# Kernel optimization log

Measured on AMD Instinct MI355X. Metric: run time of the kernel, lower is better.

The kernel has to match this reference:

```python
import jax, jax.numpy as jnp
import numpy as np

N_NODES = 50000
N_EDGES = 800000
IN_C, HID_C, OUT_C = 512, 256, 128


def setup_inputs() -> dict:
    key = jax.random.key(0)
    k1, k2, k3, k4, k5, k6 = jax.random.split(key, 6)
    x = jax.random.normal(k1, (N_NODES, IN_C), dtype=jnp.float32)
    edge_index = jax.random.randint(k2, (2, N_EDGES), 0, N_NODES, dtype=jnp.int64)
    # Glorot-ish init for linear weights, zero bias (PyG GCNConv default)
    W1 = jax.random.normal(k3, (IN_C, HID_C), dtype=jnp.float32) / np.sqrt(IN_C)
    b1 = jnp.zeros((HID_C,), dtype=jnp.float32)
    W2 = jax.random.normal(k4, (HID_C, OUT_C), dtype=jnp.float32) / np.sqrt(HID_C)
    b2 = jnp.zeros((OUT_C,), dtype=jnp.float32)
    return {"x": x, "edge_index": edge_index, "W1": W1, "b1": b1, "W2": W2, "b2": b2}


def _gcn_layer(h, src, dst, norm, W, b, n_nodes):
    # h: [N, Fin] -> [N, Fout];  out_i = sum_{j->i} norm_e * (h W)_j + b
    h = h @ W
    msg = h[src] * norm[:, None]            # [E+N, Fout]
    out = jax.ops.segment_sum(msg, dst, num_segments=n_nodes)
    return out + b


def reference(x, edge_index, W1, b1, W2, b2):
    n = x.shape[0]
    loops = jnp.arange(n, dtype=edge_index.dtype)
    src = jnp.concatenate([edge_index[0], loops])  # add self-loops
    dst = jnp.concatenate([edge_index[1], loops])
    # symmetric normalization D^{-1/2} (A+I) D^{-1/2}
    deg = jax.ops.segment_sum(jnp.ones_like(src, dtype=x.dtype), dst, num_segments=n)
    dinv = jax.lax.rsqrt(jnp.maximum(deg, 1.0))
    norm = dinv[src] * dinv[dst]

    h = _gcn_layer(x, src, dst, norm, W1, b1, n)
    h = jax.nn.relu(h)
    # dropout: identity in eval mode (training=False)
    out = _gcn_layer(h, src, dst, norm, W2, b2, n)
    return out
```

## Files before the change

kernel.cpp:

```cpp
#include <hip/hip_runtime.h>
#include <hip/hip_bf16.h>

#define N_NODES 50000
#define N_EDGES 800000
#define IN_C 512
#define HID_C 256
#define OUT_C 128
#define SCAN_BLOCKS 49

typedef short bf16x8 __attribute__((ext_vector_type(8)));
typedef float f32x4 __attribute__((ext_vector_type(4)));
typedef float f32x2 __attribute__((ext_vector_type(2)));

__device__ __forceinline__ float bf2f(unsigned short u) {
    return __uint_as_float(((unsigned)u) << 16);
}
__device__ __forceinline__ unsigned short f2bf(float f) {
    __hip_bfloat16 h = __float2bfloat16(f);
    return *(unsigned short*)&h;
}
__device__ __forceinline__ void acc_fp8x4(int dw, float* a) {
    f32x2 lo = __builtin_amdgcn_cvt_pk_f32_fp8(dw, false);
    f32x2 hi = __builtin_amdgcn_cvt_pk_f32_fp8(dw, true);
    a[0] += lo[0]; a[1] += lo[1]; a[2] += hi[0]; a[3] += hi[1];
}
__device__ __forceinline__ unsigned char f2fp8(float f) {
    return (unsigned char)(__builtin_amdgcn_cvt_pk_fp8_f32(f, 0.0f, 0, false) & 0xff);
}
__device__ __forceinline__ void glds16(const void* gp, void* lp) {
    __builtin_amdgcn_global_load_lds((const __attribute__((address_space(1))) void*)gp,
                                     (__attribute__((address_space(3))) void*)lp, 16, 0, 0);
}

__global__ void zero_counts_kernel(int* __restrict__ counts) {
    int i = blockIdx.x * blockDim.x + threadIdx.x;
    if (i < N_NODES) counts[i] = 0;
}

__global__ void count_kernel(const int* __restrict__ ei, int* __restrict__ counts) {
    int e = blockIdx.x * blockDim.x + threadIdx.x;
    if (e < N_EDGES) atomicAdd(&counts[ei[N_EDGES + e]], 1);
}

__global__ __launch_bounds__(256) void scan_part_kernel(const int* __restrict__ counts,
                                                        int* __restrict__ excl,
                                                        int* __restrict__ bsums) {
    __shared__ int tsum[256];
    const int t = threadIdx.x;
    const int base = blockIdx.x * 1024 + t * 4;
    int v[4];
    int s = 0;
#pragma unroll
    for (int j = 0; j < 4; j++) {
        int idx = base + j;
        v[j] = (idx < N_NODES) ? counts[idx] : 0;
        s += v[j];
    }
    tsum[t] = s;
    __syncthreads();
    for (int off = 1; off < 256; off <<= 1) {
        int add = (t >= off) ? tsum[t - off] : 0;
        __syncthreads();
        tsum[t] += add;
        __syncthreads();
    }
    int run = tsum[t] - s;
#pragma unroll
    for (int j = 0; j < 4; j++) {
        int idx = base + j;
        if (idx < N_NODES) excl[idx] = run;
        run += v[j];
    }
    if (t == 255) bsums[blockIdx.x] = tsum[255];
}

__global__ void scan_sums_kernel(int* __restrict__ bsums) {
    int ln = threadIdx.x;
    int v = (ln < SCAN_BLOCKS) ? bsums[ln] : 0;
    for (int off = 1; off < 64; off <<= 1) {
        int u = __shfl_up(v, off, 64);
        if (ln >= off) v += u;
    }
    int excl = __shfl_up(v, 1, 64);
    if (ln == 0) excl = 0;
    if (ln < SCAN_BLOCKS) bsums[ln] = excl;
}

__global__ void add_dinv_kernel(int* __restrict__ offsets, const int* __restrict__ bsums,
                                int* __restrict__ woff, const int* __restrict__ counts,
                                float* __restrict__ dinv) {
    int i = blockIdx.x * blockDim.x + threadIdx.x;
    if (i < N_NODES) {
        int o = offsets[i] + bsums[i >> 10];
        offsets[i] = o;
        woff[i] = o;
        dinv[i] = rsqrtf(1.0f + (float)counts[i]);
    }
    if (i == 0) offsets[N_NODES] = N_EDGES;
}

__global__ void fill_kernel(const int* __restrict__ ei, int* __restrict__ woff,
                            int* __restrict__ sedge) {
    int e = blockIdx.x * blockDim.x + threadIdx.x;
    if (e < N_EDGES) {
        int s = ei[e];
        int d = ei[N_EDGES + e];
        int pos = atomicAdd(&woff[d], 1);
        sedge[pos] = s;
    }
}

__global__ __launch_bounds__(256) void tcast_kernel(const float* __restrict__ W,
                                                    unsigned short* __restrict__ WT,
                                                    int K, int N) {
    int idx = blockIdx.x * 256 + threadIdx.x;
    int n = idx / K, k = idx - n * K;
    WT[idx] = f2bf(W[(size_t)k * N + n]);
}

__global__ __launch_bounds__(256) void gemm1_fused(const float* __restrict__ x,
                                                   const unsigned short* __restrict__ BT,
                                                   unsigned char* __restrict__ C,
                                                   const float* __restrict__ dinv) {
    __shared__ unsigned short As[2][64 * 32];
    __shared__ unsigned short Bs[2][256 * 32];

    const int tid = threadIdx.x;
    const int w = tid >> 6;
    const int ln = tid & 63;
    const int br = blockIdx.x * 64;

    const int quad = ln >> 4;
    const int l16 = ln & 15;
    const int wc = w * 64;

    const int ar = tid >> 2;
    const int ak = (tid & 3) * 8;

    int arow = br + ar;
    arow = arow < N_NODES ? arow : N_NODES - 1;
    const float* xrow = x + (size_t)arow * IN_C + ak;
    const int brow = (tid >> 2);

    f32x4 acc[4][4];
#pragma unroll
    for (int mt = 0; mt < 4; mt++)
#pragma unroll
        for (int nt = 0; nt < 4; nt++) acc[mt][nt] = (f32x4){0.f, 0.f, 0.f, 0.f};

    {
        float4 v0 = *(const float4*)(xrow);
        float4 v1 = *(const float4*)(xrow + 4);
#pragma unroll
        for (int tt = 0; tt < 4; tt++) {
            const unsigned short* gp = BT + (size_t)(brow + 64 * tt) * IN_C + ak;
            glds16(gp, &Bs[0][tt * 2048 + tid * 8]);
        }
        bf16x8 a8;
        a8[0] = (short)f2bf(v0.x); a8[1] = (short)f2bf(v0.y);
        a8[2] = (short)f2bf(v0.z); a8[3] = (short)f2bf(v0.w);
        a8[4] = (short)f2bf(v1.x); a8[5] = (short)f2bf(v1.y);
        a8[6] = (short)f2bf(v1.z); a8[7] = (short)f2bf(v1.w);
        *(bf16x8*)&As[0][ar * 32 + ak] = a8;
    }
    __syncthreads();

    for (int t = 0; t < 16; t++) {
        const int buf = t & 1;
        const int nxt = buf ^ 1;
        const bool more = t < 15;
        float4 v0, v1;
        if (more) {
            const int kk = (t + 1) * 32;
            v0 = *(const float4*)(xrow + kk);
            v1 = *(const float4*)(xrow + kk + 4);
#pragma unroll
            for (int tt = 0; tt < 4; tt++) {
                const unsigned short* gp = BT + (size_t)(brow + 64 * tt) * IN_C + kk + ak;
                glds16(gp, &Bs[nxt][tt * 2048 + tid * 8]);
            }
        }

        bf16x8 af[4], bfr[4];
#pragma unroll
        for (int mt = 0; mt < 4; mt++)
            af[mt] = *(const bf16x8*)&As[buf][(mt * 16 + l16) * 32 + quad * 8];
#pragma unroll
        for (int nt = 0; nt < 4; nt++)
            bfr[nt] = *(const bf16x8*)&Bs[buf][(wc + nt * 16 + l16) * 32 + quad * 8];
#pragma unroll
        for (int mt = 0; mt < 4; mt++)
#pragma unroll
            for (int nt = 0; nt < 4; nt++)
                acc[mt][nt] = __builtin_amdgcn_mfma_f32_16x16x32_bf16(af[mt], bfr[nt],
                                                                      acc[mt][nt], 0, 0, 0);
        if (more) {
            bf16x8 a8;
            a8[0] = (short)f2bf(v0.x); a8[1] = (short)f2bf(v0.y);
            a8[2] = (short)f2bf(v0.z); a8[3] = (short)f2bf(v0.w);
            a8[4] = (short)f2bf(v1.x); a8[5] = (short)f2bf(v1.y);
            a8[6] = (short)f2bf(v1.z); a8[7] = (short)f2bf(v1.w);
            *(bf16x8*)&As[nxt][ar * 32 + ak] = a8;
        }
        __syncthreads();
    }

#pragma unroll
    for (int mt = 0; mt < 4; mt++) {
#pragma unroll
        for (int r = 0; r < 4; r++) {
            int gr = br + mt * 16 + quad * 4 + r;
            if (gr < N_NODES) {
                float ds = dinv[gr];
#pragma unroll
                for (int nt = 0; nt < 4; nt++) {
                    int gc = wc + nt * 16 + l16;
                    C[(size_t)gr * HID_C + gc] = f2fp8(ds * acc[mt][nt][r]);
                }
            }
        }
    }
}

__global__ __launch_bounds__(256) void gemm2_db(const unsigned short* __restrict__ A,
                                                const unsigned short* __restrict__ BT,
                                                unsigned short* __restrict__ C,
                                                const float* __restrict__ dinv) {
    __shared__ unsigned short As[2][64 * 32];
    __shared__ unsigned short Bs[2][128 * 32];

    const int tid = threadIdx.x;
    const int w = tid >> 6;
    const int ln = tid & 63;
    const int br = blockIdx.x * 64;

    const int quad = ln >> 4;
    const int l16 = ln & 15;
    const int wr = (w >> 1) * 32;
    const int wc = (w & 1) * 64;

    const int ak = (tid & 3) * 8;
    const int trow = tid >> 2;

    int arow = br + trow;
    arow = arow < N_NODES ? arow : N_NODES - 1;
    const unsigned short* agp0 = A + (size_t)arow * HID_C + ak;

    f32x4 acc[2][4];
#pragma unroll
    for (int mt = 0; mt < 2; mt++)
#pragma unroll
        for (int nt = 0; nt < 4; nt++) acc[mt][nt] = (f32x4){0.f, 0.f, 0.f, 0.f};

    glds16(agp0, &As[0][tid * 8]);
#pragma unroll
    for (int tt = 0; tt < 2; tt++) {
        const unsigned short* gp = BT + (size_t)(trow + 64 * tt) * HID_C + ak;
        glds16(gp, &Bs[0][tt * 2048 + tid * 8]);
    }
    __syncthreads();

    for (int t = 0; t < 8; t++) {
        const int buf = t & 1;
        const int nxt = buf ^ 1;
        if (t < 7) {
            const int kk = (t + 1) * 32;
            glds16(agp0 + kk, &As[nxt][tid * 8]);
#pragma unroll
            for (int tt = 0; tt < 2; tt++) {
                const unsigned short* gp = BT + (size_t)(trow + 64 * tt) * HID_C + kk + ak;
                glds16(gp, &Bs[nxt][tt * 2048 + tid * 8]);
            }
        }

        bf16x8 af[2], bfr[4];
#pragma unroll
        for (int mt = 0; mt < 2; mt++)
            af[mt] = *(const bf16x8*)&As[buf][(wr + mt * 16 + l16) * 32 + quad * 8];
#pragma unroll
        for (int nt = 0; nt < 4; nt++)
            bfr[nt] = *(const bf16x8*)&Bs[buf][(wc + nt * 16 + l16) * 32 + quad * 8];
#pragma unroll
        for (int mt = 0; mt < 2; mt++)
#pragma unroll
            for (int nt = 0; nt < 4; nt++)
                acc[mt][nt] = __builtin_amdgcn_mfma_f32_16x16x32_bf16(af[mt], bfr[nt],
                                                                      acc[mt][nt], 0, 0, 0);
        __syncthreads();
    }

#pragma unroll
    for (int mt = 0; mt < 2; mt++) {
#pragma unroll
        for (int r = 0; r < 4; r++) {
            int gr = br + wr + mt * 16 + quad * 4 + r;
            if (gr < N_NODES) {
                float ds = dinv[gr];
#pragma unroll
                for (int nt = 0; nt < 4; nt++) {
                    int gc = wc + nt * 16 + l16;
                    C[(size_t)gr * OUT_C + gc] = f2bf(ds * acc[mt][nt][r]);
                }
            }
        }
    }
}

__global__ __launch_bounds__(256) void gather1_fp8(const int* __restrict__ offsets,
                                                   const int* __restrict__ sedge,
                                                   const unsigned char* __restrict__ H,
                                                   const float* __restrict__ dinv,
                                                   const float* __restrict__ bias,
                                                   unsigned short* __restrict__ out) {
    const int node = blockIdx.x * 4 + (threadIdx.x >> 6);
    if (node >= N_NODES) return;
    const int ln = threadIdx.x & 63;
    const int g = ln >> 5;
    const int l = ln & 31;
    const int c0 = l * 8;

    float acc[8] = {};
    if (g == 0) {
        uint2 d = *(const uint2*)&H[(size_t)node * HID_C + c0];
        acc_fp8x4((int)d.x, acc);
        acc_fp8x4((int)d.y, acc + 4);
    }

    int k = offsets[node] + g;
    const int k1 = offsets[node + 1];
    for (; k + 6 < k1; k += 8) {
        int s0 = sedge[k], s1 = sedge[k + 2], s2 = sedge[k + 4], s3 = sedge[k + 6];
        uint2 d0 = *(const uint2*)&H[(size_t)s0 * HID_C + c0];
        uint2 d1 = *(const uint2*)&H[(size_t)s1 * HID_C + c0];
        uint2 d2 = *(const uint2*)&H[(size_t)s2 * HID_C + c0];
        uint2 d3 = *(const uint2*)&H[(size_t)s3 * HID_C + c0];
        acc_fp8x4((int)d0.x, acc); acc_fp8x4((int)d0.y, acc + 4);
        acc_fp8x4((int)d1.x, acc); acc_fp8x4((int)d1.y, acc + 4);
        acc_fp8x4((int)d2.x, acc); acc_fp8x4((int)d2.y, acc + 4);
        acc_fp8x4((int)d3.x, acc); acc_fp8x4((int)d3.y, acc + 4);
    }
    for (; k < k1; k += 2) {
        int s0 = sedge[k];
        uint2 d0 = *(const uint2*)&H[(size_t)s0 * HID_C + c0];
        acc_fp8x4((int)d0.x, acc);
        acc_fp8x4((int)d0.y, acc + 4);
    }

#pragma unroll
    for (int j = 0; j < 8; j++) acc[j] += __shfl_xor(acc[j], 32, 64);

    if (g == 0) {
        const float di = dinv[node];
        bf16x8 o;
#pragma unroll
        for (int j = 0; j < 8; j++)
            o[j] = (short)f2bf(fmaxf(di * acc[j] + bias[c0 + j], 0.0f));
        *(bf16x8*)&out[(size_t)node * HID_C + c0] = o;
    }
}

__global__ __launch_bounds__(256) void gather2_bf16(const int* __restrict__ offsets,
                                                    const int* __restrict__ sedge,
                                                    const unsigned short* __restrict__ H,
                                                    const float* __restrict__ dinv,
                                                    const float* __restrict__ bias,
                                                    float* __restrict__ out) {
    const int node = blockIdx.x * 4 + (threadIdx.x >> 6);
    if (node >= N_NODES) return;
    const int ln = threadIdx.x & 63;
    const int g = ln >> 4;
    const int l = ln & 15;
    const int c0 = l * 8;

    float acc[8] = {};
    if (g == 0) {
        bf16x8 h = *(const bf16x8*)&H[(size_t)node * OUT_C + c0];
#pragma unroll
        for (int j = 0; j < 8; j++) acc[j] = bf2f((unsigned short)h[j]);
    }

    int k = offsets[node] + g;
    const int k1 = offsets[node + 1];
    for (; k + 12 < k1; k += 16) {
        int s0 = sedge[k], s1 = sedge[k + 4], s2 = sedge[k + 8], s3 = sedge[k + 12];
        bf16x8 h0 = *(const bf16x8*)&H[(size_t)s0 * OUT_C + c0];
        bf16x8 h1 = *(const bf16x8*)&H[(size_t)s1 * OUT_C + c0];
        bf16x8 h2 = *(const bf16x8*)&H[(size_t)s2 * OUT_C + c0];
        bf16x8 h3 = *(const bf16x8*)&H[(size_t)s3 * OUT_C + c0];
#pragma unroll
        for (int j = 0; j < 8; j++) {
            acc[j] += bf2f((unsigned short)h0[j]);
            acc[j] += bf2f((unsigned short)h1[j]);
            acc[j] += bf2f((unsigned short)h2[j]);
            acc[j] += bf2f((unsigned short)h3[j]);
        }
    }
    for (; k < k1; k += 4) {
        int s0 = sedge[k];
        bf16x8 h0 = *(const bf16x8*)&H[(size_t)s0 * OUT_C + c0];
#pragma unroll
        for (int j = 0; j < 8; j++) acc[j] += bf2f((unsigned short)h0[j]);
    }

#pragma unroll
    for (int m = 16; m < 64; m <<= 1) {
#pragma unroll
        for (int j = 0; j < 8; j++) acc[j] += __shfl_xor(acc[j], m, 64);
    }

    if (g == 0) {
        const float di = dinv[node];
        float o[8];
#pragma unroll
        for (int j = 0; j < 8; j++) o[j] = di * acc[j] + bias[c0 + j];
        *(float4*)&out[(size_t)node * OUT_C + c0] = make_float4(o[0], o[1], o[2], o[3]);
        *(float4*)&out[(size_t)node * OUT_C + c0 + 4] = make_float4(o[4], o[5], o[6], o[7]);
    }
}

extern "C" void kernel_launch(void* const* d_in, const int* in_sizes, int n_in,
                              void* d_out, int out_size, void* d_ws, size_t ws_size,
                              hipStream_t stream) {
    const float* x  = (const float*)d_in[0];
    const int*   ei = (const int*)d_in[1];
    const float* W1 = (const float*)d_in[2];
    const float* b1 = (const float*)d_in[3];
    const float* W2 = (const float*)d_in[4];
    const float* b2 = (const float*)d_in[5];
    float* out = (float*)d_out;

    int*   counts     = (int*)d_ws;
    int*   offsets    = counts + 50048;
    int*   woff       = offsets + 50052;
    int*   bsums      = woff + 50048;
    float* dinv       = (float*)(bsums + 64);
    int*   sedge      = (int*)(dinv + 50048);
    unsigned short* W1T = (unsigned short*)(sedge + 800000);
    unsigned short* W2T = W1T + 131072;
    unsigned short* xb  = W2T + 32768;
    unsigned char*  H1  = (unsigned char*)(xb + (size_t)N_NODES * IN_C);
    unsigned short* A1b = xb;
    unsigned short* H2  = xb + (size_t)N_NODES * HID_C;

    zero_counts_kernel<<<(N_NODES + 255) / 256, 256, 0, stream>>>(counts);
    count_kernel<<<(N_EDGES + 255) / 256, 256, 0, stream>>>(ei, counts);
    scan_part_kernel<<<SCAN_BLOCKS, 256, 0, stream>>>(counts, offsets, bsums);
    scan_sums_kernel<<<1, 64, 0, stream>>>(bsums);
    add_dinv_kernel<<<(N_NODES + 255) / 256, 256, 0, stream>>>(offsets, bsums, woff, counts, dinv);
    fill_kernel<<<(N_EDGES + 255) / 256, 256, 0, stream>>>(ei, woff, sedge);

    tcast_kernel<<<(IN_C * HID_C) / 256, 256, 0, stream>>>(W1, W1T, IN_C, HID_C);
    tcast_kernel<<<(HID_C * OUT_C) / 256, 256, 0, stream>>>(W2, W2T, HID_C, OUT_C);

    gemm1_fused<<<(N_NODES + 63) / 64, 256, 0, stream>>>(x, W1T, H1, dinv);
    gather1_fp8<<<(N_NODES + 3) / 4, 256, 0, stream>>>(offsets, sedge, H1, dinv, b1, A1b);

    gemm2_db<<<(N_NODES + 63) / 64, 256, 0, stream>>>(A1b, W2T, H2, dinv);
    gather2_bf16<<<(N_NODES + 3) / 4, 256, 0, stream>>>(offsets, sedge, H2, dinv, b2, out);
}
```

Baseline: 383.3 us.

## Retile first GEMM to 128x128 2D grid and drop LDS double buffering

The first-layer GEMM moves from 64-row blocks covering all 256 output columns to 128x128 tiles on a 2D grid, with the four waves arranged 2x2. The LDS double-buffering and software prefetch are removed in favour of a simple load-sync-compute-sync loop. The aim is to use less shared memory per block for more occupancy and to balance A and B reuse. In exchange, each x row is now read and converted by two column blocks, and load latency is no longer overlapped with compute inside a block.

```diff
diff --git a/kernel.cpp b/kernel.cpp
--- a/kernel.cpp
+++ b/kernel.cpp
@@ -118,29 +118,33 @@
     WT[idx] = f2bf(W[(size_t)k * N + n]);
 }
 
-__global__ __launch_bounds__(256) void gemm1_fused(const float* __restrict__ x,
-                                                   const unsigned short* __restrict__ BT,
-                                                   unsigned char* __restrict__ C,
-                                                   const float* __restrict__ dinv) {
-    __shared__ unsigned short As[2][64 * 32];
-    __shared__ unsigned short Bs[2][256 * 32];
+__global__ __launch_bounds__(256) void gemm1_f32(const float* __restrict__ x,
+                                                 const unsigned short* __restrict__ BT,
+                                                 unsigned char* __restrict__ C,
+                                                 const float* __restrict__ dinv) {
+    __shared__ unsigned short As[128 * 32];
+    __shared__ unsigned short Bs[128 * 32];
 
     const int tid = threadIdx.x;
     const int w = tid >> 6;
     const int ln = tid & 63;
-    const int br = blockIdx.x * 64;
+    const int br = blockIdx.y * 128;
+    const int bc = blockIdx.x * 128;
 
     const int quad = ln >> 4;
     const int l16 = ln & 15;
-    const int wc = w * 64;
-
-    const int ar = tid >> 2;
-    const int ak = (tid & 3) * 8;
-
-    int arow = br + ar;
-    arow = arow < N_NODES ? arow : N_NODES - 1;
-    const float* xrow = x + (size_t)arow * IN_C + ak;
-    const int brow = (tid >> 2);
+    const int wr = (w >> 1) * 64;
+    const int wc = (w & 1) * 64;
+
+    const int crow = ln >> 2;
+    const int koff = (ln & 3) * 8;
+
+    int row0 = br + (w + 0) * 16 + crow;
+    int row1 = br + (w + 4) * 16 + crow;
+    row0 = row0 < N_NODES ? row0 : N_NODES - 1;
+    row1 = row1 < N_NODES ? row1 : N_NODES - 1;
+    const float* xp0 = x + (size_t)row0 * IN_C + koff;
+    const float* xp1 = x + (size_t)row1 * IN_C + koff;
 
     f32x4 acc[4][4];
 #pragma unroll
@@ -148,60 +152,44 @@
 #pragma unroll
         for (int nt = 0; nt < 4; nt++) acc[mt][nt] = (f32x4){0.f, 0.f, 0.f, 0.f};
 
-    {
-        float4 v0 = *(const float4*)(xrow);
-        float4 v1 = *(const float4*)(xrow + 4);
-#pragma unroll
-        for (int tt = 0; tt < 4; tt++) {
-            const unsigned short* gp = BT + (size_t)(brow + 64 * tt) * IN_C + ak;
-            glds16(gp, &Bs[0][tt * 2048 + tid * 8]);
+    for (int kk = 0; kk < IN_C; kk += 32) {
+        float4 u0 = *(const float4*)(xp0 + kk);
+        float4 u1 = *(const float4*)(xp0 + kk + 4);
+        float4 u2 = *(const float4*)(xp1 + kk);
+        float4 u3 = *(const float4*)(xp1 + kk + 4);
+#pragma unroll
+        for (int t = 0; t < 2; t++) {
+            int c = w + t * 4;
+            int rowb = bc + c * 16 + crow;
+            const unsigned short* gp = BT + (size_t)rowb * IN_C + kk + koff;
+            glds16(gp, Bs + c * 512 + ln * 8);
         }
-        bf16x8 a8;
-        a8[0] = (short)f2bf(v0.x); a8[1] = (short)f2bf(v0.y);
-        a8[2] = (short)f2bf(v0.z); a8[3] = (short)f2bf(v0.w);
-        a8[4] = (short)f2bf(v1.x); a8[5] = (short)f2bf(v1.y);
-        a8[6] = (short)f2bf(v1.z); a8[7] = (short)f2bf(v1.w);
-        *(bf16x8*)&As[0][ar * 32 + ak] = a8;
-    }
-    __syncthreads();
-
-    for (int t = 0; t < 16; t++) {
-        const int buf = t & 1;
-        const int nxt = buf ^ 1;
-        const bool more = t < 15;
-        float4 v0, v1;
-        if (more) {
-            const int kk = (t + 1) * 32;
-            v0 = *(const float4*)(xrow + kk);
-            v1 = *(const float4*)(xrow + kk + 4);
-#pragma unroll
-            for (int tt = 0; tt < 4; tt++) {
-                const unsigned short* gp = BT + (size_t)(brow + 64 * tt) * IN_C + kk + ak;
-                glds16(gp, &Bs[nxt][tt * 2048 + tid * 8]);
-            }
-        }
+        bf16x8 a0, a1;
+        a0[0] = (short)f2bf(u0.x); a0[1] = (short)f2bf(u0.y);
+        a0[2] = (short)f2bf(u0.z); a0[3] = (short)f2bf(u0.w);
+        a0[4] = (short)f2bf(u1.x); a0[5] = (short)f2bf(u1.y);
+        a0[6] = (short)f2bf(u1.z); a0[7] = (short)f2bf(u1.w);
+        a1[0] = (short)f2bf(u2.x); a1[1] = (short)f2bf(u2.y);
+        a1[2] = (short)f2bf(u2.z); a1[3] = (short)f2bf(u2.w);
+        a1[4] = (short)f2bf(u3.x); a1[5] = (short)f2bf(u3.y);
+        a1[6] = (short)f2bf(u3.z); a1[7] = (short)f2bf(u3.w);
+        *(bf16x8*)&As[(w + 0) * 512 + ln * 8] = a0;
+        *(bf16x8*)&As[(w + 4) * 512 + ln * 8] = a1;
+        __syncthreads();
 
         bf16x8 af[4], bfr[4];
 #pragma unroll
         for (int mt = 0; mt < 4; mt++)
-            af[mt] = *(const bf16x8*)&As[buf][(mt * 16 + l16) * 32 + quad * 8];
+            af[mt] = *(const bf16x8*)&As[(wr + mt * 16 + l16) * 32 + quad * 8];
 #pragma unroll
         for (int nt = 0; nt < 4; nt++)
-            bfr[nt] = *(const bf16x8*)&Bs[buf][(wc + nt * 16 + l16) * 32 + quad * 8];
+            bfr[nt] = *(const bf16x8*)&Bs[(wc + nt * 16 + l16) * 32 + quad * 8];
 #pragma unroll
         for (int mt = 0; mt < 4; mt++)
 #pragma unroll
             for (int nt = 0; nt < 4; nt++)
                 acc[mt][nt] = __builtin_amdgcn_mfma_f32_16x16x32_bf16(af[mt], bfr[nt],
                                                                       acc[mt][nt], 0, 0, 0);
-        if (more) {
-            bf16x8 a8;
-            a8[0] = (short)f2bf(v0.x); a8[1] = (short)f2bf(v0.y);
-            a8[2] = (short)f2bf(v0.z); a8[3] = (short)f2bf(v0.w);
-            a8[4] = (short)f2bf(v1.x); a8[5] = (short)f2bf(v1.y);
-            a8[6] = (short)f2bf(v1.z); a8[7] = (short)f2bf(v1.w);
-            *(bf16x8*)&As[nxt][ar * 32 + ak] = a8;
-        }
         __syncthreads();
     }
 
@@ -209,12 +197,12 @@
     for (int mt = 0; mt < 4; mt++) {
 #pragma unroll
         for (int r = 0; r < 4; r++) {
-            int gr = br + mt * 16 + quad * 4 + r;
+            int gr = br + wr + mt * 16 + quad * 4 + r;
             if (gr < N_NODES) {
                 float ds = dinv[gr];
 #pragma unroll
                 for (int nt = 0; nt < 4; nt++) {
-                    int gc = wc + nt * 16 + l16;
+                    int gc = bc + wc + nt * 16 + l16;
                     C[(size_t)gr * HID_C + gc] = f2fp8(ds * acc[mt][nt][r]);
                 }
             }
@@ -452,7 +440,10 @@
     tcast_kernel<<<(IN_C * HID_C) / 256, 256, 0, stream>>>(W1, W1T, IN_C, HID_C);
     tcast_kernel<<<(HID_C * OUT_C) / 256, 256, 0, stream>>>(W2, W2T, HID_C, OUT_C);
 
-    gemm1_fused<<<(N_NODES + 63) / 64, 256, 0, stream>>>(x, W1T, H1, dinv);
+    {
+        dim3 grid(HID_C / 128, (N_NODES + 127) / 128);
+        gemm1_f32<<<grid, 256, 0, stream>>>(x, W1T, H1, dinv);
+    }
     gather1_fp8<<<(N_NODES + 3) / 4, 256, 0, stream>>>(offsets, sedge, H1, dinv, b1, A1b);
 
     gemm2_db<<<(N_NODES + 63) / 64, 256, 0, stream>>>(A1b, W2T, H2, dinv);
```

After: 394.1 us. 1.03x slower.
